# Kernel tuning notes

Measured on AMD Instinct MI355X. Metric: run time of the kernel, lower is better.

Reference implementation:

```python
import jax, jax.numpy as jnp
import numpy as np

HEADS = 4
NEG_SLOPE = 0.2  # PyG GATConv default
LN_EPS = 1e-5


def setup_inputs() -> dict:
    key = jax.random.key(0)
    ks = jax.random.split(key, 12)
    N, D, E = 30000, 128, 480000
    s = 1.0 / np.sqrt(D)
    return {
        "x": jax.random.normal(ks[0], (N, D), dtype=jnp.float32),
        "edge_index": jax.random.randint(ks[1], (2, E), 0, N, dtype=jnp.int64),
        "W_gat": jax.random.normal(ks[2], (HEADS, D, D), dtype=jnp.float32) * s,
        "att_src": jax.random.normal(ks[3], (HEADS, D), dtype=jnp.float32) * s,
        "att_dst": jax.random.normal(ks[4], (HEADS, D), dtype=jnp.float32) * s,
        "b_gat": jnp.zeros((D,), dtype=jnp.float32),
        "W_gcn": jax.random.normal(ks[5], (D, D), dtype=jnp.float32) * s,
        "b_gcn": jnp.zeros((D,), dtype=jnp.float32),
        "W_gate": jax.random.normal(ks[6], (2 * D, 2), dtype=jnp.float32) * (1.0 / np.sqrt(2 * D)),
        "b_gate": jnp.zeros((2,), dtype=jnp.float32),
        "gamma": jnp.ones((D,), dtype=jnp.float32),
        "beta": jnp.zeros((D,), dtype=jnp.float32),
    }


def reference(x, edge_index, W_gat, att_src, att_dst, b_gat, W_gcn, b_gcn,
              W_gate, b_gate, gamma, beta):
    N, D = x.shape
    # Both PyG GATConv and GCNConv add self-loops by default.
    loops = jnp.arange(N, dtype=edge_index.dtype)
    src = jnp.concatenate([edge_index[0], loops])  # message source j
    dst = jnp.concatenate([edge_index[1], loops])  # message target i

    # ---- GATConv (heads=4, concat=False -> mean over heads), eval (no dropout) ----
    xh = jnp.einsum('nd,hdf->nhf', x, W_gat)            # [N, H, D]
    a_s = jnp.einsum('nhf,hf->nh', xh, att_src)         # [N, H]
    a_d = jnp.einsum('nhf,hf->nh', xh, att_dst)         # [N, H]
    e = jax.nn.leaky_relu(a_s[src] + a_d[dst], NEG_SLOPE)  # [E', H]
    # segment softmax over incoming edges of each destination node
    m = jax.ops.segment_max(e, dst, num_segments=N)     # every node has a self-loop
    alpha = jnp.exp(e - m[dst])
    denom = jax.ops.segment_sum(alpha, dst, num_segments=N)
    alpha = alpha / denom[dst]                          # [E', H]
    # aggregate per head (fixed small loop keeps peak memory at E*D per head)
    gat_acc = jnp.zeros((N, D), dtype=x.dtype)
    for h in range(HEADS):
        msg = alpha[:, h:h + 1] * xh[:, h, :][src]      # [E', D]
        gat_acc = gat_acc + jax.ops.segment_sum(msg, dst, num_segments=N)
    gat_out = gat_acc / HEADS + b_gat

    xg = x @ W_gcn                                      # [N, D]
    deg = jax.ops.segment_sum(jnp.ones_like(src, dtype=x.dtype), dst, num_segments=N)
    dinv = jnp.where(deg > 0, jax.lax.rsqrt(deg), 0.0)
    coef = dinv[src] * dinv[dst]                        # [E']
    gcn_out = jax.ops.segment_sum(coef[:, None] * xg[src], dst, num_segments=N) + b_gcn

    # ---- gated fusion + residual + LayerNorm ----
    gate = jax.nn.softmax(jnp.concatenate([gat_out, gcn_out], axis=-1) @ W_gate + b_gate, axis=-1)
    fused = gate[:, 0:1] * gat_out + gate[:, 1:2] * gcn_out
    h = fused + gat_out
    mu = jnp.mean(h, axis=-1, keepdims=True)
    var = jnp.mean((h - mu) ** 2, axis=-1, keepdims=True)
    return (h - mu) * jax.lax.rsqrt(var + LN_EPS) * gamma + beta
```

## Files before the change

kernel.cpp:

```cpp
#include <hip/hip_runtime.h>
#include <hip/hip_bf16.h>

#define D 128
#define NH 4
#define NEG_SLOPE 0.2f
#define LN_EPS 1e-5f

typedef __attribute__((ext_vector_type(4))) float f32x4;
typedef __attribute__((ext_vector_type(8))) short bf16x8;

__device__ __forceinline__ float bf2f(unsigned short u) {
  union { unsigned int i; float f; } c; c.i = ((unsigned int)u) << 16; return c.f;
}
__device__ __forceinline__ unsigned short f2bf(float f) {
  union { float f; unsigned int i; } c; c.f = f;
  unsigned int r = c.i + 0x7FFFu + ((c.i >> 16) & 1u);
  return (unsigned short)(r >> 16);
}

__global__ __launch_bounds__(128) void k_prep(
    const float* __restrict__ Wgat, const float* __restrict__ Wgcn,
    const float* __restrict__ att_src, const float* __restrict__ att_dst,
    unsigned short* __restrict__ Wt2g, unsigned short* __restrict__ Wt2c,
    float* __restrict__ wtil_s, float* __restrict__ wtil_d,
    int* __restrict__ deg, int N)
{
  int c = blockIdx.x, t = threadIdx.x;
  if (c < 128) {
    #pragma unroll
    for (int i = 0; i < 4; ++i) {
      int k = t + i * 128;
      int h = k >> 7, kk = k & 127;
      Wt2g[c * 512 + k] = f2bf(Wgat[((size_t)h * D + kk) * D + c]);
    }
  } else if (c < 256) {
    int cc = c - 128;
    Wt2c[cc * 128 + t] = f2bf(Wgcn[(size_t)t * D + cc]);
  } else if (c < 264) {
    int b2 = c - 256;
    int h = b2 >> 1, which = b2 & 1;
    const float* av = (which ? att_dst : att_src) + h * D;
    const float* Wrow = Wgat + ((size_t)h * D + t) * D;
    float s = 0.f;
    for (int f = 0; f < D; ++f) s += Wrow[f] * av[f];
    (which ? wtil_d : wtil_s)[h * D + t] = s;
  } else {
    int i = (c - 264) * 128 + t;
    if (i < N) deg[i] = 0;
  }
}

__global__ __launch_bounds__(256) void k_xb_deg(
    const float* __restrict__ x,
    const float* __restrict__ wtil_s, const float* __restrict__ wtil_d,
    unsigned short* __restrict__ xb, float* __restrict__ a_s, float* __restrict__ a_d,
    const int* __restrict__ ei, int* __restrict__ deg,
    int N, int E, int NBN)
{
  if ((int)blockIdx.x >= NBN) {
    int e = (blockIdx.x - NBN) * 256 + threadIdx.x;
    if (e < E + N) {
      int dst = (e < E) ? ei[E + e] : (e - E);
      atomicAdd(&deg[dst], 1);
    }
    return;
  }
  const int w = threadIdx.x >> 6, l = threadIdx.x & 63;
  const int n = blockIdx.x * 4 + w;
  if (n >= N) return;
  float2 xv = ((const float2*)(x + (size_t)n * D))[l];
  ushort2 p; p.x = f2bf(xv.x); p.y = f2bf(xv.y);
  *(ushort2*)(xb + (size_t)n * D + 2 * l) = p;
  float s0 = xv.x * wtil_s[2*l]       + xv.y * wtil_s[2*l+1];
  float s1 = xv.x * wtil_s[D+2*l]     + xv.y * wtil_s[D+2*l+1];
  float s2 = xv.x * wtil_s[2*D+2*l]   + xv.y * wtil_s[2*D+2*l+1];
  float s3 = xv.x * wtil_s[3*D+2*l]   + xv.y * wtil_s[3*D+2*l+1];
  float d0 = xv.x * wtil_d[2*l]       + xv.y * wtil_d[2*l+1];
  float d1 = xv.x * wtil_d[D+2*l]     + xv.y * wtil_d[D+2*l+1];
  float d2 = xv.x * wtil_d[2*D+2*l]   + xv.y * wtil_d[2*D+2*l+1];
  float d3 = xv.x * wtil_d[3*D+2*l]   + xv.y * wtil_d[3*D+2*l+1];
  #pragma unroll
  for (int off = 32; off; off >>= 1) {
    s0 += __shfl_xor(s0, off); s1 += __shfl_xor(s1, off);
    s2 += __shfl_xor(s2, off); s3 += __shfl_xor(s3, off);
    d0 += __shfl_xor(d0, off); d1 += __shfl_xor(d1, off);
    d2 += __shfl_xor(d2, off); d3 += __shfl_xor(d3, off);
  }
  if (l == 0) {
    ((float4*)a_s)[n] = make_float4(s0, s1, s2, s3);
    ((float4*)a_d)[n] = make_float4(d0, d1, d2, d3);
  }
}

__global__ void k_scan1(const int* __restrict__ deg, int N, int* __restrict__ bsum)
{
  __shared__ int s[256];
  int t = threadIdx.x;
  int i = blockIdx.x * 256 + t;
  s[t] = (i < N) ? deg[i] : 0;
  __syncthreads();
  for (int off = 128; off; off >>= 1) {
    if (t < off) s[t] += s[t + off];
    __syncthreads();
  }
  if (t == 0) bsum[blockIdx.x] = s[0];
}

__global__ void k_scan3(const int* __restrict__ deg, const int* __restrict__ bsum,
                        int nb, int N, int Et, int* __restrict__ row_ptr,
                        int* __restrict__ cursor, float* __restrict__ dinv)
{
  __shared__ int s[256];
  __shared__ int r[256];
  const int t = threadIdx.x, b = blockIdx.x;
  const int i = b * 256 + t;
  const int v = (i < N) ? deg[i] : 0;
  s[t] = v;
  r[t] = (t < b && t < nb) ? bsum[t] : 0;
  __syncthreads();
  for (int off = 1; off < 256; off <<= 1) {
    int xv = (t >= off) ? s[t - off] : 0;
    __syncthreads();
    s[t] += xv;
    __syncthreads();
  }
  for (int off = 128; off; off >>= 1) {
    if (t < off) r[t] += r[t + off];
    __syncthreads();
  }
  const int base = r[0];
  if (i < N) {
    int excl = base + s[t] - v;
    row_ptr[i] = excl;
    cursor[i] = excl;
    dinv[i] = rsqrtf((float)v);
  }
  if (i == 0) row_ptr[N] = Et;
}

__global__ void k_fill(const int* __restrict__ ei, int E, int N,
                       int* __restrict__ cursor, int* __restrict__ col_src)
{
  int e = blockIdx.x * blockDim.x + threadIdx.x;
  if (e >= E + N) return;
  int src, dst;
  if (e < E) { src = ei[e]; dst = ei[E + e]; }
  else       { src = e - E; dst = src; }
  int pos = atomicAdd(&cursor[dst], 1);
  col_src[pos] = src;
}

#define ACC_EDGE(AL, CF, XV) do {                                        \
    float fa_[4] = {bf2f(XV.x), bf2f(XV.y), bf2f(XV.z), bf2f(XV.w)};     \
    float aa_[4] = {AL.x, AL.y, AL.z, AL.w};                             \
    _Pragma("unroll") for (int h_ = 0; h_ < 4; ++h_)                     \
      _Pragma("unroll") for (int d_ = 0; d_ < 4; ++d_)                   \
        ug[h_][d_] += aa_[h_] * fa_[d_];                                 \
    _Pragma("unroll") for (int d_ = 0; d_ < 4; ++d_)                     \
      vg[d_] += (CF) * fa_[d_];                                          \
  } while (0)

__global__ __launch_bounds__(256) void k_agg2(
    const unsigned short* __restrict__ xb,
    const float* __restrict__ a_s, const float* __restrict__ a_d,
    const int* __restrict__ row_ptr, const int* __restrict__ col_src,
    const float* __restrict__ dinv,
    unsigned short* __restrict__ UV, int N)
{
  __shared__ float4 sh_al[8][40];
  __shared__ int    sh_src[8][40];
  __shared__ float  sh_cf[8][40];
  const int hw = threadIdx.x >> 5, lh = threadIdx.x & 31;
  const int n = blockIdx.x * 8 + hw;
  if (n >= N) return;
  const int start = row_ptr[n], end = row_ptr[n + 1];
  const float4 adn = ((const float4*)a_d)[n];

  float den0 = 0.f, den1 = 0.f, den2 = 0.f, den3 = 0.f;
  float ug[4][4] = {};
  float vg[4] = {};

  for (int base = start; base < end; base += 32) {
    const int cnt = min(32, end - base);
    if (lh < cnt) {
      int s = col_src[base + lh];
      float4 as4 = ((const float4*)a_s)[s];
      float e0 = as4.x + adn.x; e0 = (e0 >= 0.f) ? e0 : NEG_SLOPE * e0;
      float e1 = as4.y + adn.y; e1 = (e1 >= 0.f) ? e1 : NEG_SLOPE * e1;
      float e2 = as4.z + adn.z; e2 = (e2 >= 0.f) ? e2 : NEG_SLOPE * e2;
      float e3 = as4.w + adn.w; e3 = (e3 >= 0.f) ? e3 : NEG_SLOPE * e3;
      float x0 = __expf(e0), x1 = __expf(e1), x2 = __expf(e2), x3 = __expf(e3);
      den0 += x0; den1 += x1; den2 += x2; den3 += x3;
      sh_al[hw][lh] = make_float4(x0, x1, x2, x3);
      sh_src[hw][lh] = s;
      sh_cf[hw][lh] = dinv[s];
    }
    if (lh < 7) {
      sh_al[hw][cnt + lh] = make_float4(0.f, 0.f, 0.f, 0.f);
      sh_src[hw][cnt + lh] = 0;
      sh_cf[hw][cnt + lh] = 0.f;
    }
    for (int j = 0; j < cnt; j += 8) {
      ushort4 xv[8];
      float4 al[8];
      float cf[8];
      #pragma unroll
      for (int u = 0; u < 8; ++u) {
        int s = sh_src[hw][j + u];
        xv[u] = *(const ushort4*)(xb + ((size_t)s << 7) + (lh << 2));
      }
      #pragma unroll
      for (int u = 0; u < 8; ++u) {
        al[u] = sh_al[hw][j + u];
        cf[u] = sh_cf[hw][j + u];
      }
      #pragma unroll
      for (int u = 0; u < 8; ++u) ACC_EDGE(al[u], cf[u], xv[u]);
    }
  }

  #pragma unroll
  for (int off = 16; off; off >>= 1) {
    den0 += __shfl_xor(den0, off); den1 += __shfl_xor(den1, off);
    den2 += __shfl_xor(den2, off); den3 += __shfl_xor(den3, off);
  }
  const float r[4] = {1.f / den0, 1.f / den1, 1.f / den2, 1.f / den3};
  const float dn = dinv[n];
  unsigned short* uvp = UV + (size_t)n * 640;
  #pragma unroll
  for (int h = 0; h < 4; ++h) {
    ushort4 u;
    u.x = f2bf(ug[h][0] * r[h]); u.y = f2bf(ug[h][1] * r[h]);
    u.z = f2bf(ug[h][2] * r[h]); u.w = f2bf(ug[h][3] * r[h]);
    *(ushort4*)(uvp + h * 128 + 4 * lh) = u;
  }
  ushort4 v4;
  v4.x = f2bf(vg[0] * dn); v4.y = f2bf(vg[1] * dn);
  v4.z = f2bf(vg[2] * dn); v4.w = f2bf(vg[3] * dn);
  *(ushort4*)(uvp + 512 + 4 * lh) = v4;
}

__global__ __launch_bounds__(256) void k_gemm3(
    const unsigned short* __restrict__ UV,
    const unsigned short* __restrict__ Wt2g, const unsigned short* __restrict__ Wt2c,
    const float* __restrict__ b_gat, const float* __restrict__ b_gcn,
    const float* __restrict__ W_gate, const float* __restrict__ b_gate,
    const float* __restrict__ gamma, const float* __restrict__ beta,
    float* __restrict__ out, int N)
{
  __shared__ unsigned short As[64 * 128];
  __shared__ unsigned short Bs[128 * 128];
  __shared__ float ec[8][128];
  const int t = threadIdx.x;
  const int m0 = blockIdx.x * 64;

  {
    int idx = t * 4;
    #pragma unroll
    for (int i = 0; i < 4; ++i) {
      int arr = (idx + i) >> 7, c = (idx + i) & 127;
      float v;
      switch (arr) {
        case 0: v = b_gat[c]; break;
        case 1: v = b_gcn[c]; break;
        case 2: v = W_gate[2 * c]; break;
        case 3: v = W_gate[2 * c + 1]; break;
        case 4: v = W_gate[256 + 2 * c]; break;
        case 5: v = W_gate[256 + 2 * c + 1]; break;
        case 6: v = gamma[c]; break;
        default: v = beta[c]; break;
      }
      ec[arr][c] = v;
    }
  }

  const int w = t >> 6, l = t & 63;
  const int lrow = l & 15, lk = l >> 4;
  const int arow = w * 16 + lrow;

  f32x4 accg[8], accc[8];
  #pragma unroll
  for (int n = 0; n < 8; ++n) {
    accg[n] = (f32x4){0.f, 0.f, 0.f, 0.f};
    accc[n] = (f32x4){0.f, 0.f, 0.f, 0.f};
  }

  for (int kc = 0; kc < 5; ++kc) {
    const int abase = (kc < 4) ? kc * 128 : 512;
    __syncthreads();
    #pragma unroll
    for (int i = 0; i < 4; ++i) {
      int g = i * 256 + t;
      int row = g >> 4, kb = g & 15;
      int gr = m0 + row;
      uint4 v = make_uint4(0u, 0u, 0u, 0u);
      if (gr < N) v = *(const uint4*)(UV + (size_t)gr * 640 + abase + kb * 8);
      *(uint4*)&As[row * 128 + ((kb ^ (row & 7)) << 3)] = v;
    }
    #pragma unroll
    for (int i = 0; i < 8; ++i) {
      int g = i * 256 + t;
      int col = g >> 4, kb = g & 15;
      uint4 v = (kc < 4)
        ? *(const uint4*)(Wt2g + (size_t)col * 512 + kc * 128 + kb * 8)
        : *(const uint4*)(Wt2c + (size_t)col * 128 + kb * 8);
      *(uint4*)&Bs[col * 128 + ((kb ^ (col & 7)) << 3)] = v;
    }
    __syncthreads();
    f32x4* acc = (kc < 4) ? accg : accc;
    #pragma unroll
    for (int ks = 0; ks < 4; ++ks) {
      int kb = ks * 4 + lk;
      bf16x8 a = *(const bf16x8*)&As[arow * 128 + ((kb ^ (arow & 7)) << 3)];
      #pragma unroll
      for (int n = 0; n < 8; ++n) {
        int col = n * 16 + lrow;
        bf16x8 b = *(const bf16x8*)&Bs[col * 128 + ((kb ^ (col & 7)) << 3)];
        acc[n] = __builtin_amdgcn_mfma_f32_16x16x32_bf16(a, b, acc[n], 0, 0, 0);
      }
    }
  }

  const float bg0 = b_gate[0], bg1 = b_gate[1];
  #pragma unroll
  for (int j = 0; j < 4; ++j) {
    const int r = m0 + w * 16 + lk * 4 + j;
    float ga[8], gc[8];
    float z0 = 0.f, z1 = 0.f;
    #pragma unroll
    for (int n = 0; n < 8; ++n) {
      int c = n * 16 + lrow;
      ga[n] = accg[n][j] * 0.25f + ec[0][c];
      gc[n] = accc[n][j] + ec[1][c];
      z0 += ga[n] * ec[2][c] + gc[n] * ec[4][c];
      z1 += ga[n] * ec[3][c] + gc[n] * ec[5][c];
    }
    #pragma unroll
    for (int off = 8; off; off >>= 1) { z0 += __shfl_xor(z0, off); z1 += __shfl_xor(z1, off); }
    z0 += bg0; z1 += bg1;
    float mz = fmaxf(z0, z1);
    float e0 = __expf(z0 - mz), e1 = __expf(z1 - mz);
    float inv = 1.f / (e0 + e1);
    float w0 = e0 * inv, w1 = e1 * inv;
    float h[8], ss = 0.f;
    #pragma unroll
    for (int n = 0; n < 8; ++n) { h[n] = (1.f + w0) * ga[n] + w1 * gc[n]; ss += h[n]; }
    #pragma unroll
    for (int off = 8; off; off >>= 1) ss += __shfl_xor(ss, off);
    float mu = ss * (1.f / 128.f);
    float vs = 0.f;
    #pragma unroll
    for (int n = 0; n < 8; ++n) { h[n] -= mu; vs += h[n] * h[n]; }
    #pragma unroll
    for (int off = 8; off; off >>= 1) vs += __shfl_xor(vs, off);
    float rstd = rsqrtf(vs * (1.f / 128.f) + LN_EPS);
    if (r < N) {
      #pragma unroll
      for (int n = 0; n < 8; ++n) {
        int c = n * 16 + lrow;
        out[(size_t)r * 128 + c] = h[n] * rstd * ec[6][c] + ec[7][c];
      }
    }
  }
}

extern "C" void kernel_launch(void* const* d_in, const int* in_sizes, int n_in,
                              void* d_out, int out_size, void* d_ws, size_t ws_size,
                              hipStream_t stream)
{
  const float* x       = (const float*)d_in[0];
  const int*   ei      = (const int*)d_in[1];
  const float* Wgat    = (const float*)d_in[2];
  const float* att_src = (const float*)d_in[3];
  const float* att_dst = (const float*)d_in[4];
  const float* b_gat   = (const float*)d_in[5];
  const float* Wgcn    = (const float*)d_in[6];
  const float* b_gcn   = (const float*)d_in[7];
  const float* W_gate  = (const float*)d_in[8];
  const float* b_gate  = (const float*)d_in[9];
  const float* gamma   = (const float*)d_in[10];
  const float* beta    = (const float*)d_in[11];
  float* out = (float*)d_out;

  const int N  = in_sizes[0] / D;
  const int E  = in_sizes[1] / 2;
  const int Et = E + N;

  char* p = (char*)d_ws;
  unsigned short* xb   = (unsigned short*)p; p += (size_t)N * D * 2;
  unsigned short* UV   = (unsigned short*)p; p += (size_t)N * 640 * 2;
  unsigned short* Wt2g = (unsigned short*)p; p += (size_t)128 * 512 * 2;
  unsigned short* Wt2c = (unsigned short*)p; p += (size_t)128 * 128 * 2;
  float* wtil_s  = (float*)p; p += 512 * 4;
  float* wtil_d  = (float*)p; p += 512 * 4;
  float* a_s     = (float*)p; p += (size_t)N * NH * 4;
  float* a_d     = (float*)p; p += (size_t)N * NH * 4;
  float* dinv    = (float*)p; p += (size_t)N * 4;
  int* deg       = (int*)p;   p += (size_t)N * 4;
  int* row_ptr   = (int*)p;   p += (size_t)(N + 1) * 4;
  int* cursor    = (int*)p;   p += (size_t)N * 4;
  int* col_src   = (int*)p;   p += (size_t)Et * 4;
  int* bsum      = (int*)p;   p += 1024;

  const int NBN = (N + 3) / 4;
  const int NBE = (Et + 255) / 256;
  const int nzb = (N + 127) / 128;
  const int nb  = (N + 255) / 256;

  k_prep<<<264 + nzb, 128, 0, stream>>>(
      Wgat, Wgcn, att_src, att_dst, Wt2g, Wt2c, wtil_s, wtil_d, deg, N);
  k_xb_deg<<<NBN + NBE, 256, 0, stream>>>(x, wtil_s, wtil_d, xb, a_s, a_d,
                                           ei, deg, N, E, NBN);
  k_scan1<<<nb, 256, 0, stream>>>(deg, N, bsum);
  k_scan3<<<nb, 256, 0, stream>>>(deg, bsum, nb, N, Et, row_ptr, cursor, dinv);
  k_fill<<<NBE, 256, 0, stream>>>(ei, E, N, cursor, col_src);
  k_agg2<<<(N + 7) / 8, 256, 0, stream>>>(xb, a_s, a_d, row_ptr, col_src, dinv, UV, N);
  k_gemm3<<<(N + 63) / 64, 256, 0, stream>>>(UV, Wt2g, Wt2c, b_gat, b_gcn,
                                              W_gate, b_gate, gamma, beta, out, N);
  (void)n_in; (void)out_size; (void)ws_size;
}
```

Measured before the change: 126.6 us.

## Fuse preprocessing, CSR build and aggregation into one cooperative kernel

Measured after the change: 373.9 us. 195% more time.

```diff
diff --git a/kernel.cpp b/kernel.cpp
--- a/kernel.cpp
+++ b/kernel.cpp
@@ -1,5 +1,8 @@
 #include <hip/hip_runtime.h>
 #include <hip/hip_bf16.h>
+#include <hip/hip_cooperative_groups.h>
+
+namespace cg = cooperative_groups;
 
 #define D 128
 #define NH 4
@@ -47,6 +50,195 @@
   } else {
     int i = (c - 264) * 128 + t;
     if (i < N) deg[i] = 0;
+  }
+}
+
+#define ACC_EDGE(AL, CF, XV) do {                                        \
+    float fa_[4] = {bf2f(XV.x), bf2f(XV.y), bf2f(XV.z), bf2f(XV.w)};     \
+    float aa_[4] = {AL.x, AL.y, AL.z, AL.w};                             \
+    _Pragma("unroll") for (int h_ = 0; h_ < 4; ++h_)                     \
+      _Pragma("unroll") for (int d_ = 0; d_ < 4; ++d_)                   \
+        ug[h_][d_] += aa_[h_] * fa_[d_];                                 \
+    _Pragma("unroll") for (int d_ = 0; d_ < 4; ++d_)                     \
+      vg[d_] += (CF) * fa_[d_];                                          \
+  } while (0)
+
+__global__ __launch_bounds__(256, 4) void k_mega(
+    const float* __restrict__ x,
+    const float* __restrict__ wtil_s, const float* __restrict__ wtil_d,
+    unsigned short* __restrict__ xb, float* __restrict__ a_s, float* __restrict__ a_d,
+    const int* __restrict__ ei, int* __restrict__ deg, int* __restrict__ bsum,
+    int* __restrict__ row_ptr, int* __restrict__ cursor, float* __restrict__ dinv,
+    int* __restrict__ col_src, unsigned short* __restrict__ UV,
+    int N, int E, int Et, int NBN, int NBE, int nb, int NG)
+{
+  cg::grid_group grid = cg::this_grid();
+  const int t = threadIdx.x;
+  const int nblk = gridDim.x;
+
+  __shared__ int sA[256];
+  __shared__ int sB[256];
+  __shared__ float4 sh_al[8][40];
+  __shared__ int    sh_src[8][40];
+  __shared__ float  sh_cf[8][40];
+
+  for (int vb = blockIdx.x; vb < NBN; vb += nblk) {
+    const int w = t >> 6, l = t & 63;
+    const int n = vb * 4 + w;
+    if (n < N) {
+      float2 xv = ((const float2*)(x + (size_t)n * D))[l];
+      ushort2 p2; p2.x = f2bf(xv.x); p2.y = f2bf(xv.y);
+      *(ushort2*)(xb + (size_t)n * D + 2 * l) = p2;
+      float s0 = xv.x * wtil_s[2*l]       + xv.y * wtil_s[2*l+1];
+      float s1 = xv.x * wtil_s[D+2*l]     + xv.y * wtil_s[D+2*l+1];
+      float s2 = xv.x * wtil_s[2*D+2*l]   + xv.y * wtil_s[2*D+2*l+1];
+      float s3 = xv.x * wtil_s[3*D+2*l]   + xv.y * wtil_s[3*D+2*l+1];
+      float d0 = xv.x * wtil_d[2*l]       + xv.y * wtil_d[2*l+1];
+      float d1 = xv.x * wtil_d[D+2*l]     + xv.y * wtil_d[D+2*l+1];
+      float d2 = xv.x * wtil_d[2*D+2*l]   + xv.y * wtil_d[2*D+2*l+1];
+      float d3 = xv.x * wtil_d[3*D+2*l]   + xv.y * wtil_d[3*D+2*l+1];
+      #pragma unroll
+      for (int off = 32; off; off >>= 1) {
+        s0 += __shfl_xor(s0, off); s1 += __shfl_xor(s1, off);
+        s2 += __shfl_xor(s2, off); s3 += __shfl_xor(s3, off);
+        d0 += __shfl_xor(d0, off); d1 += __shfl_xor(d1, off);
+        d2 += __shfl_xor(d2, off); d3 += __shfl_xor(d3, off);
+      }
+      if (l == 0) {
+        ((float4*)a_s)[n] = make_float4(s0, s1, s2, s3);
+        ((float4*)a_d)[n] = make_float4(d0, d1, d2, d3);
+      }
+    }
+  }
+  for (int vb = blockIdx.x; vb < NBE; vb += nblk) {
+    int e = vb * 256 + t;
+    if (e < E + N) {
+      int dst = (e < E) ? ei[E + e] : (e - E);
+      atomicAdd(&deg[dst], 1);
+    }
+  }
+  grid.sync();
+
+  for (int vb = blockIdx.x; vb < nb; vb += nblk) {
+    int i = vb * 256 + t;
+    sA[t] = (i < N) ? deg[i] : 0;
+    __syncthreads();
+    for (int off = 128; off; off >>= 1) {
+      if (t < off) sA[t] += sA[t + off];
+      __syncthreads();
+    }
+    if (t == 0) bsum[vb] = sA[0];
+    __syncthreads();
+  }
+  grid.sync();
+
+  for (int vb = blockIdx.x; vb < nb; vb += nblk) {
+    const int i = vb * 256 + t;
+    const int v = (i < N) ? deg[i] : 0;
+    sA[t] = v;
+    sB[t] = (t < vb && t < nb) ? bsum[t] : 0;
+    __syncthreads();
+    for (int off = 1; off < 256; off <<= 1) {
+      int xv = (t >= off) ? sA[t - off] : 0;
+      __syncthreads();
+      sA[t] += xv;
+      __syncthreads();
+    }
+    for (int off = 128; off; off >>= 1) {
+      if (t < off) sB[t] += sB[t + off];
+      __syncthreads();
+    }
+    const int base = sB[0];
+    if (i < N) {
+      int excl = base + sA[t] - v;
+      row_ptr[i] = excl;
+      cursor[i] = excl;
+      dinv[i] = rsqrtf((float)v);
+    }
+    if (i == 0) row_ptr[N] = Et;
+    __syncthreads();
+  }
+  grid.sync();
+
+  for (int vb = blockIdx.x; vb < NBE; vb += nblk) {
+    int e = vb * 256 + t;
+    if (e < E + N) {
+      int src, dst;
+      if (e < E) { src = ei[e]; dst = ei[E + e]; }
+      else       { src = e - E; dst = src; }
+      int pos = atomicAdd(&cursor[dst], 1);
+      col_src[pos] = src;
+    }
+  }
+  grid.sync();
+
+  for (int vb = blockIdx.x; vb < NG; vb += nblk) {
+    const int hw = t >> 5, lh = t & 31;
+    const int n = vb * 8 + hw;
+    if (n < N) {
+      const int start = row_ptr[n], end = row_ptr[n + 1];
+      const float4 adn = ((const float4*)a_d)[n];
+      float den0 = 0.f, den1 = 0.f, den2 = 0.f, den3 = 0.f;
+      float ug[4][4] = {};
+      float vg[4] = {};
+      for (int base = start; base < end; base += 32) {
+        const int cnt = min(32, end - base);
+        if (lh < cnt) {
+          int s = col_src[base + lh];
+          float4 as4 = ((const float4*)a_s)[s];
+          float e0 = as4.x + adn.x; e0 = (e0 >= 0.f) ? e0 : NEG_SLOPE * e0;
+          float e1 = as4.y + adn.y; e1 = (e1 >= 0.f) ? e1 : NEG_SLOPE * e1;
+          float e2 = as4.z + adn.z; e2 = (e2 >= 0.f) ? e2 : NEG_SLOPE * e2;
+          float e3 = as4.w + adn.w; e3 = (e3 >= 0.f) ? e3 : NEG_SLOPE * e3;
+          float x0 = __expf(e0), x1 = __expf(e1), x2 = __expf(e2), x3 = __expf(e3);
+          den0 += x0; den1 += x1; den2 += x2; den3 += x3;
+          sh_al[hw][lh] = make_float4(x0, x1, x2, x3);
+          sh_src[hw][lh] = s;
+          sh_cf[hw][lh] = dinv[s];
+        }
+        if (lh < 7) {
+          sh_al[hw][cnt + lh] = make_float4(0.f, 0.f, 0.f, 0.f);
+          sh_src[hw][cnt + lh] = 0;
+          sh_cf[hw][cnt + lh] = 0.f;
+        }
+        for (int j = 0; j < cnt; j += 8) {
+          ushort4 xv[8];
+          float4 al[8];
+          float cf[8];
+          #pragma unroll
+          for (int u = 0; u < 8; ++u) {
+            int s = sh_src[hw][j + u];
+            xv[u] = *(const ushort4*)(xb + ((size_t)s << 7) + (lh << 2));
+          }
+          #pragma unroll
+          for (int u = 0; u < 8; ++u) {
+            al[u] = sh_al[hw][j + u];
+            cf[u] = sh_cf[hw][j + u];
+          }
+          #pragma unroll
+          for (int u = 0; u < 8; ++u) ACC_EDGE(al[u], cf[u], xv[u]);
+        }
+      }
+      #pragma unroll
+      for (int off = 16; off; off >>= 1) {
+        den0 += __shfl_xor(den0, off); den1 += __shfl_xor(den1, off);
+        den2 += __shfl_xor(den2, off); den3 += __shfl_xor(den3, off);
+      }
+      const float r[4] = {1.f / den0, 1.f / den1, 1.f / den2, 1.f / den3};
+      const float dn = dinv[n];
+      unsigned short* uvp = UV + (size_t)n * 640;
+      #pragma unroll
+      for (int h = 0; h < 4; ++h) {
+        ushort4 u;
+        u.x = f2bf(ug[h][0] * r[h]); u.y = f2bf(ug[h][1] * r[h]);
+        u.z = f2bf(ug[h][2] * r[h]); u.w = f2bf(ug[h][3] * r[h]);
+        *(ushort4*)(uvp + h * 128 + 4 * lh) = u;
+      }
+      ushort4 v4;
+      v4.x = f2bf(vg[0] * dn); v4.y = f2bf(vg[1] * dn);
+      v4.z = f2bf(vg[2] * dn); v4.w = f2bf(vg[3] * dn);
+      *(ushort4*)(uvp + 512 + 4 * lh) = v4;
+    }
   }
 }
 
@@ -150,16 +342,6 @@
   col_src[pos] = src;
 }
 
-#define ACC_EDGE(AL, CF, XV) do {                                        \
-    float fa_[4] = {bf2f(XV.x), bf2f(XV.y), bf2f(XV.z), bf2f(XV.w)};     \
-    float aa_[4] = {AL.x, AL.y, AL.z, AL.w};                             \
-    _Pragma("unroll") for (int h_ = 0; h_ < 4; ++h_)                     \
-      _Pragma("unroll") for (int d_ = 0; d_ < 4; ++d_)                   \
-        ug[h_][d_] += aa_[h_] * fa_[d_];                                 \
-    _Pragma("unroll") for (int d_ = 0; d_ < 4; ++d_)                     \
-      vg[d_] += (CF) * fa_[d_];                                          \
-  } while (0)
-
 __global__ __launch_bounds__(256) void k_agg2(
     const unsigned short* __restrict__ xb,
     const float* __restrict__ a_s, const float* __restrict__ a_d,
@@ -382,9 +564,9 @@
   const float* beta    = (const float*)d_in[11];
   float* out = (float*)d_out;
 
-  const int N  = in_sizes[0] / D;
-  const int E  = in_sizes[1] / 2;
-  const int Et = E + N;
+  int N  = in_sizes[0] / D;
+  int E  = in_sizes[1] / 2;
+  int Et = E + N;
 
   char* p = (char*)d_ws;
   unsigned short* xb   = (unsigned short*)p; p += (size_t)N * D * 2;
@@ -402,19 +584,42 @@
   int* col_src   = (int*)p;   p += (size_t)Et * 4;
   int* bsum      = (int*)p;   p += 1024;
 
-  const int NBN = (N + 3) / 4;
-  const int NBE = (Et + 255) / 256;
-  const int nzb = (N + 127) / 128;
-  const int nb  = (N + 255) / 256;
+  int NBN = (N + 3) / 4;
+  int NBE = (Et + 255) / 256;
+  int nzb = (N + 127) / 128;
+  int nb  = (N + 255) / 256;
+  int NG  = (N + 7) / 8;
 
   k_prep<<<264 + nzb, 128, 0, stream>>>(
       Wgat, Wgcn, att_src, att_dst, Wt2g, Wt2c, wtil_s, wtil_d, deg, N);
-  k_xb_deg<<<NBN + NBE, 256, 0, stream>>>(x, wtil_s, wtil_d, xb, a_s, a_d,
-                                           ei, deg, N, E, NBN);
-  k_scan1<<<nb, 256, 0, stream>>>(deg, N, bsum);
-  k_scan3<<<nb, 256, 0, stream>>>(deg, bsum, nb, N, Et, row_ptr, cursor, dinv);
-  k_fill<<<NBE, 256, 0, stream>>>(ei, E, N, cursor, col_src);
-  k_agg2<<<(N + 7) / 8, 256, 0, stream>>>(xb, a_s, a_d, row_ptr, col_src, dinv, UV, N);
+
+  int maxB = 0;
+  hipError_t oerr = hipOccupancyMaxActiveBlocksPerMultiprocessor(
+      &maxB, (const void*)k_mega, 256, 0);
+  int grid = (oerr == hipSuccess && maxB > 0) ? maxB * 256 : 512;
+  if (grid > 2048) grid = 2048;
+  int maxwork = NBE;
+  if (NBN > maxwork) maxwork = NBN;
+  if (NG > maxwork) maxwork = NG;
+  if (grid > maxwork) grid = maxwork;
+
+  void* args[] = {
+    (void*)&x, (void*)&wtil_s, (void*)&wtil_d, (void*)&xb, (void*)&a_s, (void*)&a_d,
+    (void*)&ei, (void*)&deg, (void*)&bsum, (void*)&row_ptr, (void*)&cursor,
+    (void*)&dinv, (void*)&col_src, (void*)&UV,
+    (void*)&N, (void*)&E, (void*)&Et, (void*)&NBN, (void*)&NBE, (void*)&nb, (void*)&NG
+  };
+  hipError_t lerr = hipLaunchCooperativeKernel(
+      (void*)k_mega, dim3(grid), dim3(256), args, 0, stream);
+  if (lerr != hipSuccess) {
+    k_xb_deg<<<NBN + NBE, 256, 0, stream>>>(x, wtil_s, wtil_d, xb, a_s, a_d,
+                                             ei, deg, N, E, NBN);
+    k_scan1<<<nb, 256, 0, stream>>>(deg, N, bsum);
+    k_scan3<<<nb, 256, 0, stream>>>(deg, bsum, nb, N, Et, row_ptr, cursor, dinv);
+    k_fill<<<NBE, 256, 0, stream>>>(ei, E, N, cursor, col_src);
+    k_agg2<<<NG, 256, 0, stream>>>(xb, a_s, a_d, row_ptr, col_src, dinv, UV, N);
+  }
+
   k_gemm3<<<(N + 63) / 64, 256, 0, stream>>>(UV, Wt2g, Wt2c, b_gat, b_gcn,
                                               W_gate, b_gate, gamma, beta, out, N);
   (void)n_in; (void)out_size; (void)ws_size;
```
